# Kernel tuning notes

Measured on AMD Instinct MI355X. Metric: run time of the kernel, lower is better.

Reference implementation:

```python
import jax, jax.numpy as jnp
import numpy as np

NUM_HEADS = 16
HEAD_CH = 64
D_MODEL = 1024  # == NUM_HEADS*HEAD_CH -> out_mapper is Identity


def setup_inputs() -> dict:
    key = jax.random.key(0)
    k1, k2, k3 = jax.random.split(key, 3)
    tokens = jax.random.normal(k1, (2, 2048, D_MODEL), dtype=jnp.float32)
    w_qkv = jax.random.normal(k2, (D_MODEL, 3 * D_MODEL), dtype=jnp.float32) * (1.0 / np.sqrt(D_MODEL))
    b_qkv = jax.random.normal(k3, (3 * D_MODEL,), dtype=jnp.float32) * 0.02
    return {"tokens": tokens, "w_qkv": w_qkv, "b_qkv": b_qkv}


def reference(tokens, w_qkv, b_qkv):
    b, n, _ = tokens.shape
    qkv = tokens @ w_qkv + b_qkv  # [b, n, 3*inner]
    q, k, v = jnp.split(qkv, 3, axis=-1)

    def heads(x):  # [b, n, h*d] -> [b, h, n, d]
        return x.reshape(b, n, NUM_HEADS, HEAD_CH).transpose(0, 2, 1, 3)

    q, k, v = heads(q), heads(k), heads(v)
    scores = jnp.einsum('bhqd,bhkd->bhqk', q, k) / jnp.sqrt(jnp.float32(HEAD_CH))
    attn = jax.nn.softmax(scores, axis=-1)
    out = jnp.einsum('bhqk,bhkd->bhqd', attn, v)  # [b, h, n, d]
    out = out.transpose(0, 2, 1, 3).reshape(b, n, NUM_HEADS * HEAD_CH)
    return out  # out_mapper is Identity since inner_channels == input_channels
```

## Files before the change

kernel.cpp:

```cpp
#include <hip/hip_runtime.h>
#include <stdint.h>

typedef __attribute__((ext_vector_type(8))) short shortx8;
typedef __attribute__((ext_vector_type(4))) float floatx4;
typedef unsigned short bf16_t;

#define NH 16
#define HD 64
#define SEQ 2048
#define BATCH 2
#define DM 1024
#define DM3 3072

#define GLDS(gp, lp) __builtin_amdgcn_global_load_lds( \
    (const __attribute__((address_space(1))) unsigned int*)(gp), \
    (__attribute__((address_space(3))) unsigned int*)(lp), 16, 0, 0)

__device__ __forceinline__ bf16_t f2bf(float f) {
    unsigned int u = __float_as_uint(f);
    u += 0x7fff + ((u >> 16) & 1);
    return (bf16_t)(u >> 16);
}

__global__ __launch_bounds__(256) void conv_tokens(const float* __restrict__ in,
                                                   bf16_t* __restrict__ out) {
    int idx = blockIdx.x * 256 + threadIdx.x;
    float4 a = ((const float4*)in)[idx * 2];
    float4 b = ((const float4*)in)[idx * 2 + 1];
    uint4 o;
    o.x = (unsigned)f2bf(a.x) | ((unsigned)f2bf(a.y) << 16);
    o.y = (unsigned)f2bf(a.z) | ((unsigned)f2bf(a.w) << 16);
    o.z = (unsigned)f2bf(b.x) | ((unsigned)f2bf(b.y) << 16);
    o.w = (unsigned)f2bf(b.z) | ((unsigned)f2bf(b.w) << 16);
    ((uint4*)out)[idx] = o;
}

__global__ __launch_bounds__(256) void conv_w(const float* __restrict__ w,
                                              bf16_t* __restrict__ wt) {
    __shared__ bf16_t t[64 * 65];
    const int n0 = blockIdx.x * 64;
    const int k0 = blockIdx.y * 64;
    const int tid = threadIdx.x;
    for (int i = 0; i < 16; i++) {
        int idx = i * 256 + tid;
        int r = idx >> 6, c = idx & 63;
        t[r * 65 + c] = f2bf(w[(k0 + r) * DM3 + n0 + c]);
    }
    __syncthreads();
    for (int i = 0; i < 16; i++) {
        int idx = i * 256 + tid;
        int r = idx >> 6, c = idx & 63;
        wt[(n0 + r) * DM + k0 + c] = t[c * 65 + r];
    }
}


#define QSCALE 0.18033688011f
__global__ __launch_bounds__(256) void qkv_gemm(const bf16_t* __restrict__ A,
                                                const bf16_t* __restrict__ Bt,
                                                const float* __restrict__ bias,
                                                bf16_t* __restrict__ Qo,
                                                bf16_t* __restrict__ Ko,
                                                bf16_t* __restrict__ Vto) {
    __shared__ __align__(16) char smem[128 * 136 * 2];
    bf16_t* As = (bf16_t*)smem;
    bf16_t* Bs = As + 128 * 64;
    bf16_t* Cs = (bf16_t*)smem;
    const int m0 = blockIdx.x * 128;
    const int n0 = blockIdx.y * 128;
    const int tid = threadIdx.x;
    const int wave = tid >> 6, lane = tid & 63;
    const int quad = lane >> 4, l16 = lane & 15;
    const int wm = (wave & 1) * 64, wn = (wave >> 1) * 64;
    const int srow = tid >> 3;
    const int swz8 = ((tid & 7) ^ (srow & 7)) * 8;
    const int h3 = l16 & 7;
    floatx4 acc[4][4] = {};

    for (int kt = 0; kt < DM; kt += 64) {
        __syncthreads();
        for (int rr = 0; rr < 4; rr++) {
            GLDS(&A[(m0 + rr * 32 + srow) * DM + kt + swz8], &As[rr * 2048 + tid * 8]);
            GLDS(&Bt[(n0 + rr * 32 + srow) * DM + kt + swz8], &Bs[rr * 2048 + tid * 8]);
        }
        __syncthreads();
        for (int ks = 0; ks < 2; ks++) {
            const int g = ((ks * 4 + quad) ^ h3) * 8;
            shortx8 af[4], bfr[4];
            for (int t = 0; t < 4; t++)
                af[t] = *(const shortx8*)&As[(wm + t * 16 + l16) * 64 + g];
            for (int t = 0; t < 4; t++)
                bfr[t] = *(const shortx8*)&Bs[(wn + t * 16 + l16) * 64 + g];
            for (int i = 0; i < 4; i++)
                for (int j = 0; j < 4; j++)
                    acc[i][j] = __builtin_amdgcn_mfma_f32_16x16x32_bf16(af[i], bfr[j], acc[i][j], 0, 0, 0);
        }
    }

    const int part = n0 >> 10;
    const int b = m0 >> 11, pos0 = m0 & 2047;

    if (part != 2) {
        for (int i = 0; i < 4; i++)
            for (int j = 0; j < 4; j++)
                for (int r = 0; r < 4; r++) {
                    int m = m0 + wm + i * 16 + quad * 4 + r;
                    int n = n0 + wn + j * 16 + l16;
                    float v = acc[i][j][r] + bias[n];
                    int rr = n & 1023;
                    int h = rr >> 6, d = rr & 63;
                    int pos = m & 2047;
                    if (part == 0)
                        Qo[((b * NH + h) * SEQ + pos) * HD + d] = f2bf(v * QSCALE);
                    else
                        Ko[((b * NH + h) * SEQ + pos) * HD + d] = f2bf(v);
                }
    } else {
        __syncthreads();
        for (int i = 0; i < 4; i++)
            for (int j = 0; j < 4; j++) {
                int nl = wn + j * 16 + l16;
                int n = n0 + nl;
                float bv = bias[n];
                uint2 pk;
                pk.x = (unsigned)f2bf(acc[i][j][0] + bv) | ((unsigned)f2bf(acc[i][j][1] + bv) << 16);
                pk.y = (unsigned)f2bf(acc[i][j][2] + bv) | ((unsigned)f2bf(acc[i][j][3] + bv) << 16);
                *(uint2*)&Cs[nl * 136 + wm + i * 16 + quad * 4] = pk;
            }
        __syncthreads();
        for (int p = 0; p < 8; p++) {
            int nl = p * 16 + (tid >> 4);
            int g = tid & 15;
            uint4 v = *(const uint4*)&Cs[nl * 136 + g * 8];
            int rr = (n0 + nl) & 1023;
            int h = rr >> 6, d = rr & 63;
            *(uint4*)&Vto[(size_t)((b * NH + h) * HD + d) * SEQ + pos0 + g * 8] = v;
        }
    }
}

__global__ __launch_bounds__(256, 2) void attn(const bf16_t* __restrict__ Q,
                                               const bf16_t* __restrict__ K,
                                               const bf16_t* __restrict__ Vt,
                                               float* __restrict__ out) {
    __shared__ __align__(16) char smem[65536];
    bf16_t* Ks = (bf16_t*)smem;
    bf16_t* Vs = (bf16_t*)(smem + 16384);
    bf16_t* Ps = (bf16_t*)(smem + 32768);

    const int qt_blk = blockIdx.x;
    const int bh = blockIdx.y;
    const int b = bh >> 4, h = bh & 15;
    const int q0 = qt_blk * 128;
    const bf16_t* Qb = Q + ((size_t)bh * SEQ + q0) * HD;
    const bf16_t* Kb = K + (size_t)bh * SEQ * HD;
    const bf16_t* Vb = Vt + (size_t)bh * HD * SEQ;
    const int tid = threadIdx.x;
    const int wave = tid >> 6, lane = tid & 63;
    const int quad = lane >> 4, l16 = lane & 15;
    const int h3 = l16 & 7;
    const int qh = wave >> 1, kh = wave & 1;
    bf16_t* Pw = Ps + wave * 4096;

    const int srow = tid >> 3;
    const int sg8 = ((tid & 7) ^ (srow & 7)) * 8;
    const int vrow = tid >> 4;
    const int vg8 = (((tid & 15) ^ vrow) & 15) * 8;

    shortx8 qf[4][2];
    for (int qt = 0; qt < 4; qt++)
        for (int kc = 0; kc < 2; kc++)
            qf[qt][kc] = *(const shortx8*)&Qb[(qh * 64 + qt * 16 + l16) * 64 + kc * 32 + quad * 8];

    float m_i[4] = {-1e30f, -1e30f, -1e30f, -1e30f};
    float l_i[4] = {0.f, 0.f, 0.f, 0.f};
    floatx4 acc_o[4][4] = {};

    for (int it = 0; it < SEQ / 128; ++it) {
        const int k0 = it * 128;
        for (int rr = 0; rr < 4; rr++) {
            GLDS(&Kb[(k0 + rr * 32 + srow) * 64 + sg8], &Ks[rr * 2048 + tid * 8]);
            GLDS(&Vb[(size_t)(rr * 16 + vrow) * SEQ + k0 + vg8], &Vs[rr * 2048 + tid * 8]);
        }
        __syncthreads();

        floatx4 s[4][4] = {};
        for (int kc = 0; kc < 2; kc++) {
            const int g = ((kc * 4 + quad) ^ h3) * 8;
            shortx8 kf[4];
            for (int kt = 0; kt < 4; kt++)
                kf[kt] = *(const shortx8*)&Ks[(kh * 64 + kt * 16 + l16) * 64 + g];
            for (int kt = 0; kt < 4; kt++)
                for (int qt = 0; qt < 4; qt++)
                    s[kt][qt] = __builtin_amdgcn_mfma_f32_16x16x32_bf16(kf[kt], qf[qt][kc], s[kt][qt], 0, 0, 0);
        }

        for (int qt = 0; qt < 4; qt++) {
            float mx = -1e30f;
            for (int kt = 0; kt < 4; kt++)
                for (int r = 0; r < 4; r++) mx = fmaxf(mx, s[kt][qt][r]);
            mx = fmaxf(mx, __shfl_xor(mx, 16, 64));
            mx = fmaxf(mx, __shfl_xor(mx, 32, 64));
            float mnew = fmaxf(m_i[qt], mx);
            float al = __builtin_amdgcn_exp2f(m_i[qt] - mnew);
            m_i[qt] = mnew;
            float rs = 0.f;
            for (int kt = 0; kt < 4; kt++) {
                unsigned u[4];
                for (int r = 0; r < 4; r++) {
                    float p = __builtin_amdgcn_exp2f(s[kt][qt][r] - mnew);
                    rs += p;
                    u[r] = __float_as_uint(p) + 0x8000u;
                }
                uint2 pk;
                pk.x = __builtin_amdgcn_perm(u[1], u[0], 0x07060302u);
                pk.y = __builtin_amdgcn_perm(u[3], u[2], 0x07060302u);
                *(uint2*)&Pw[(qt * 16 + l16) * 64 +
                             ((2 * kt + (quad >> 1)) ^ h3) * 8 + (quad & 1) * 4] = pk;
            }
            rs += __shfl_xor(rs, 16, 64);
            rs += __shfl_xor(rs, 32, 64);
            l_i[qt] = l_i[qt] * al + rs;
            if (__any(al < 1.0f))
                for (int dt = 0; dt < 4; dt++)
                    for (int r = 0; r < 4; r++) acc_o[dt][qt][r] *= al;
        }

        for (int kc = 0; kc < 2; kc++) {
            const int gp = ((kc * 4 + quad) ^ h3) * 8;
            shortx8 vf[4], pf[4];
            for (int qt = 0; qt < 4; qt++)
                pf[qt] = *(const shortx8*)&Pw[(qt * 16 + l16) * 64 + gp];
            for (int dt = 0; dt < 4; dt++)
                vf[dt] = *(const shortx8*)&Vs[(dt * 16 + l16) * 128 +
                                              (((kh * 8 + kc * 4 + quad) ^ l16) & 15) * 8];
            for (int dt = 0; dt < 4; dt++)
                for (int qt = 0; qt < 4; qt++)
                    acc_o[dt][qt] = __builtin_amdgcn_mfma_f32_16x16x32_bf16(vf[dt], pf[qt], acc_o[dt][qt], 0, 0, 0);
        }
        __syncthreads();
    }

    float* Osh = (float*)smem;
    float* ml = (float*)(smem + 64512);
    if (kh == 1) {
        for (int qt = 0; qt < 4; qt++) {
            for (int dt = 0; dt < 4; dt++) {
                float4 o;
                o.x = acc_o[dt][qt][0]; o.y = acc_o[dt][qt][1];
                o.z = acc_o[dt][qt][2]; o.w = acc_o[dt][qt][3];
                *(float4*)&Osh[qh * 4096 + (qt * 16 + l16) * 64 +
                               (((dt * 4 + quad) ^ l16) & 15) * 4] = o;
            }
            if (quad == 0) {
                ml[(qh * 4 + qt) * 32 + l16] = m_i[qt];
                ml[(qh * 4 + qt) * 32 + 16 + l16] = l_i[qt];
            }
        }
    }
    __syncthreads();
    if (kh == 0) {
        for (int qt = 0; qt < 4; qt++) {
            float m1 = ml[(qh * 4 + qt) * 32 + l16];
            float l1 = ml[(qh * 4 + qt) * 32 + 16 + l16];
            float m = fmaxf(m_i[qt], m1);
            float a0 = __builtin_amdgcn_exp2f(m_i[qt] - m);
            float a1 = __builtin_amdgcn_exp2f(m1 - m);
            float inv = 1.0f / (l_i[qt] * a0 + l1 * a1);
            int q = q0 + qh * 64 + qt * 16 + l16;
            for (int dt = 0; dt < 4; dt++) {
                float4 o1 = *(const float4*)&Osh[qh * 4096 + (qt * 16 + l16) * 64 +
                                                 (((dt * 4 + quad) ^ l16) & 15) * 4];
                float4 o;
                o.x = (acc_o[dt][qt][0] * a0 + o1.x * a1) * inv;
                o.y = (acc_o[dt][qt][1] * a0 + o1.y * a1) * inv;
                o.z = (acc_o[dt][qt][2] * a0 + o1.z * a1) * inv;
                o.w = (acc_o[dt][qt][3] * a0 + o1.w * a1) * inv;
                *(float4*)&out[(size_t)(b * SEQ + q) * DM + h * HD + dt * 16 + quad * 4] = o;
            }
        }
    }
}

extern "C" void kernel_launch(void* const* d_in, const int* in_sizes, int n_in,
                              void* d_out, int out_size, void* d_ws, size_t ws_size,
                              hipStream_t stream) {
    const float* tokens = (const float*)d_in[0];
    const float* w = (const float*)d_in[1];
    const float* bias = (const float*)d_in[2];
    float* out = (float*)d_out;
    char* ws = (char*)d_ws;

    bf16_t* tok_bf = (bf16_t*)(ws);
    bf16_t* wt_bf  = (bf16_t*)(ws + (size_t)8 * 1024 * 1024);
    bf16_t* Qb     = (bf16_t*)(ws + (size_t)14 * 1024 * 1024);
    bf16_t* Kb     = (bf16_t*)(ws + (size_t)22 * 1024 * 1024);
    bf16_t* Vb     = (bf16_t*)(ws + (size_t)30 * 1024 * 1024);

    conv_tokens<<<2048, 256, 0, stream>>>(tokens, tok_bf);
    conv_w<<<dim3(48, 16), 256, 0, stream>>>(w, wt_bf);
    qkv_gemm<<<dim3(32, 24), 256, 0, stream>>>(tok_bf, wt_bf, bias, Qb, Kb, Vb);
    attn<<<dim3(16, 32), 256, 0, stream>>>(Qb, Kb, Vb, out);
}
```

Before: 181.3 us.

## Merge conversion kernels, vectorize QKV epilogue, and drop LDS staging in attention

The two conversion kernels become one launch. The Q/K GEMM epilogue swaps the MFMA operands so each lane writes four packed bf16 values with a vector bias load, replacing scalar stores. The attention kernel stops staging K and V through LDS and loads MFMA fragments directly from global memory, removing the per-iteration barriers. It also adds a lazy max-rescale threshold that skips most accumulator rescales, and raises occupancy hints to three blocks. The risks are uncoalesced or redundant global reads of K and V across waves, plus a small numeric change from the deferred max update.

```diff
diff --git a/kernel.cpp b/kernel.cpp
--- a/kernel.cpp
+++ b/kernel.cpp
@@ -22,40 +22,76 @@
     return (bf16_t)(u >> 16);
 }
 
-__global__ __launch_bounds__(256) void conv_tokens(const float* __restrict__ in,
-                                                   bf16_t* __restrict__ out) {
-    int idx = blockIdx.x * 256 + threadIdx.x;
-    float4 a = ((const float4*)in)[idx * 2];
-    float4 b = ((const float4*)in)[idx * 2 + 1];
-    uint4 o;
-    o.x = (unsigned)f2bf(a.x) | ((unsigned)f2bf(a.y) << 16);
-    o.y = (unsigned)f2bf(a.z) | ((unsigned)f2bf(a.w) << 16);
-    o.z = (unsigned)f2bf(b.x) | ((unsigned)f2bf(b.y) << 16);
-    o.w = (unsigned)f2bf(b.z) | ((unsigned)f2bf(b.w) << 16);
-    ((uint4*)out)[idx] = o;
-}
-
-__global__ __launch_bounds__(256) void conv_w(const float* __restrict__ w,
-                                              bf16_t* __restrict__ wt) {
+__global__ __launch_bounds__(256) void conv_all(const float* __restrict__ tokens,
+                                                bf16_t* __restrict__ tok_bf,
+                                                const float* __restrict__ w,
+                                                bf16_t* __restrict__ wt) {
     __shared__ bf16_t t[64 * 65];
-    const int n0 = blockIdx.x * 64;
-    const int k0 = blockIdx.y * 64;
+    const int bx = blockIdx.x, tid = threadIdx.x;
+    if (bx < 2048) {
+        int idx = bx * 256 + tid;
+        float4 a = ((const float4*)tokens)[idx * 2];
+        float4 b = ((const float4*)tokens)[idx * 2 + 1];
+        uint4 o;
+        o.x = (unsigned)f2bf(a.x) | ((unsigned)f2bf(a.y) << 16);
+        o.y = (unsigned)f2bf(a.z) | ((unsigned)f2bf(a.w) << 16);
+        o.z = (unsigned)f2bf(b.x) | ((unsigned)f2bf(b.y) << 16);
+        o.w = (unsigned)f2bf(b.z) | ((unsigned)f2bf(b.w) << 16);
+        ((uint4*)tok_bf)[idx] = o;
+    } else {
+        const int bw = bx - 2048;
+        const int n0 = (bw % 48) * 64, k0 = (bw / 48) * 64;
+        for (int i = 0; i < 16; i++) {
+            int idx = i * 256 + tid;
+            int r = idx >> 6, c = idx & 63;
+            t[r * 65 + c] = f2bf(w[(k0 + r) * DM3 + n0 + c]);
+        }
+        __syncthreads();
+        for (int i = 0; i < 16; i++) {
+            int idx = i * 256 + tid;
+            int r = idx >> 6, c = idx & 63;
+            wt[(n0 + r) * DM + k0 + c] = t[c * 65 + r];
+        }
+    }
+}
+
+
+#define QSCALE 0.18033688011f
+
+template<bool SW>
+__device__ __forceinline__ void kloop(const bf16_t* __restrict__ A, const bf16_t* __restrict__ Bt,
+                                      bf16_t* __restrict__ As, bf16_t* __restrict__ Bs,
+                                      int m0, int n0, floatx4 (&acc)[4][4]) {
     const int tid = threadIdx.x;
-    for (int i = 0; i < 16; i++) {
-        int idx = i * 256 + tid;
-        int r = idx >> 6, c = idx & 63;
-        t[r * 65 + c] = f2bf(w[(k0 + r) * DM3 + n0 + c]);
-    }
-    __syncthreads();
-    for (int i = 0; i < 16; i++) {
-        int idx = i * 256 + tid;
-        int r = idx >> 6, c = idx & 63;
-        wt[(n0 + r) * DM + k0 + c] = t[c * 65 + r];
-    }
-}
-
-
-#define QSCALE 0.18033688011f
+    const int wave = tid >> 6, lane = tid & 63;
+    const int quad = lane >> 4, l16 = lane & 15;
+    const int wm = (wave & 1) * 64, wn = (wave >> 1) * 64;
+    const int srow = tid >> 3;
+    const int swz8 = ((tid & 7) ^ (srow & 7)) * 8;
+    const int h3 = l16 & 7;
+    for (int kt = 0; kt < DM; kt += 64) {
+        __syncthreads();
+        for (int rr = 0; rr < 4; rr++) {
+            GLDS(&A[(m0 + rr * 32 + srow) * DM + kt + swz8], &As[rr * 2048 + tid * 8]);
+            GLDS(&Bt[(n0 + rr * 32 + srow) * DM + kt + swz8], &Bs[rr * 2048 + tid * 8]);
+        }
+        __syncthreads();
+        for (int ks = 0; ks < 2; ks++) {
+            const int g = ((ks * 4 + quad) ^ h3) * 8;
+            shortx8 af[4], bfr[4];
+            for (int t = 0; t < 4; t++)
+                af[t] = *(const shortx8*)&As[(wm + t * 16 + l16) * 64 + g];
+            for (int t = 0; t < 4; t++)
+                bfr[t] = *(const shortx8*)&Bs[(wn + t * 16 + l16) * 64 + g];
+            for (int i = 0; i < 4; i++)
+                for (int j = 0; j < 4; j++)
+                    acc[i][j] = SW
+                        ? __builtin_amdgcn_mfma_f32_16x16x32_bf16(bfr[j], af[i], acc[i][j], 0, 0, 0)
+                        : __builtin_amdgcn_mfma_f32_16x16x32_bf16(af[i], bfr[j], acc[i][j], 0, 0, 0);
+        }
+    }
+}
+
 __global__ __launch_bounds__(256) void qkv_gemm(const bf16_t* __restrict__ A,
                                                 const bf16_t* __restrict__ Bt,
                                                 const float* __restrict__ bias,
@@ -72,56 +108,37 @@
     const int wave = tid >> 6, lane = tid & 63;
     const int quad = lane >> 4, l16 = lane & 15;
     const int wm = (wave & 1) * 64, wn = (wave >> 1) * 64;
-    const int srow = tid >> 3;
-    const int swz8 = ((tid & 7) ^ (srow & 7)) * 8;
-    const int h3 = l16 & 7;
-    floatx4 acc[4][4] = {};
-
-    for (int kt = 0; kt < DM; kt += 64) {
-        __syncthreads();
-        for (int rr = 0; rr < 4; rr++) {
-            GLDS(&A[(m0 + rr * 32 + srow) * DM + kt + swz8], &As[rr * 2048 + tid * 8]);
-            GLDS(&Bt[(n0 + rr * 32 + srow) * DM + kt + swz8], &Bs[rr * 2048 + tid * 8]);
-        }
-        __syncthreads();
-        for (int ks = 0; ks < 2; ks++) {
-            const int g = ((ks * 4 + quad) ^ h3) * 8;
-            shortx8 af[4], bfr[4];
-            for (int t = 0; t < 4; t++)
-                af[t] = *(const shortx8*)&As[(wm + t * 16 + l16) * 64 + g];
-            for (int t = 0; t < 4; t++)
-                bfr[t] = *(const shortx8*)&Bs[(wn + t * 16 + l16) * 64 + g];
-            for (int i = 0; i < 4; i++)
-                for (int j = 0; j < 4; j++)
-                    acc[i][j] = __builtin_amdgcn_mfma_f32_16x16x32_bf16(af[i], bfr[j], acc[i][j], 0, 0, 0);
-        }
-    }
-
     const int part = n0 >> 10;
     const int b = m0 >> 11, pos0 = m0 & 2047;
+    floatx4 acc[4][4] = {};
 
     if (part != 2) {
-        for (int i = 0; i < 4; i++)
-            for (int j = 0; j < 4; j++)
-                for (int r = 0; r < 4; r++) {
-                    int m = m0 + wm + i * 16 + quad * 4 + r;
-                    int n = n0 + wn + j * 16 + l16;
-                    float v = acc[i][j][r] + bias[n];
-                    int rr = n & 1023;
-                    int h = rr >> 6, d = rr & 63;
-                    int pos = m & 2047;
-                    if (part == 0)
-                        Qo[((b * NH + h) * SEQ + pos) * HD + d] = f2bf(v * QSCALE);
-                    else
-                        Ko[((b * NH + h) * SEQ + pos) * HD + d] = f2bf(v);
-                }
+        kloop<true>(A, Bt, As, Bs, m0, n0, acc);
+        for (int i = 0; i < 4; i++) {
+            int m = m0 + wm + i * 16 + l16;
+            int pos = m & 2047;
+            for (int j = 0; j < 4; j++) {
+                int nb = n0 + wn + j * 16 + quad * 4;
+                float4 bv = *(const float4*)&bias[nb];
+                float v0 = acc[i][j][0] + bv.x, v1 = acc[i][j][1] + bv.y;
+                float v2 = acc[i][j][2] + bv.z, v3 = acc[i][j][3] + bv.w;
+                if (part == 0) { v0 *= QSCALE; v1 *= QSCALE; v2 *= QSCALE; v3 *= QSCALE; }
+                uint2 pk;
+                pk.x = (unsigned)f2bf(v0) | ((unsigned)f2bf(v1) << 16);
+                pk.y = (unsigned)f2bf(v2) | ((unsigned)f2bf(v3) << 16);
+                int rr = nb & 1023;
+                int h = rr >> 6, d = rr & 63;
+                bf16_t* dst = (part == 0) ? Qo : Ko;
+                *(uint2*)&dst[(size_t)((b * NH + h) * SEQ + pos) * HD + d] = pk;
+            }
+        }
     } else {
+        kloop<false>(A, Bt, As, Bs, m0, n0, acc);
         __syncthreads();
         for (int i = 0; i < 4; i++)
             for (int j = 0; j < 4; j++) {
                 int nl = wn + j * 16 + l16;
-                int n = n0 + nl;
-                float bv = bias[n];
+                float bv = bias[n0 + nl];
                 uint2 pk;
                 pk.x = (unsigned)f2bf(acc[i][j][0] + bv) | ((unsigned)f2bf(acc[i][j][1] + bv) << 16);
                 pk.y = (unsigned)f2bf(acc[i][j][2] + bv) | ((unsigned)f2bf(acc[i][j][3] + bv) << 16);
@@ -139,15 +156,12 @@
     }
 }
 
-__global__ __launch_bounds__(256, 2) void attn(const bf16_t* __restrict__ Q,
+__global__ __launch_bounds__(256, 3) void attn(const bf16_t* __restrict__ Q,
                                                const bf16_t* __restrict__ K,
                                                const bf16_t* __restrict__ Vt,
                                                float* __restrict__ out) {
-    __shared__ __align__(16) char smem[65536];
-    bf16_t* Ks = (bf16_t*)smem;
-    bf16_t* Vs = (bf16_t*)(smem + 16384);
-    bf16_t* Ps = (bf16_t*)(smem + 32768);
-
+    __shared__ __align__(16) bf16_t Ps[4][4096];
+    __shared__ float ml[256];
     const int qt_blk = blockIdx.x;
     const int bh = blockIdx.y;
     const int b = bh >> 4, h = bh & 15;
@@ -160,40 +174,29 @@
     const int quad = lane >> 4, l16 = lane & 15;
     const int h3 = l16 & 7;
     const int qh = wave >> 1, kh = wave & 1;
-    bf16_t* Pw = Ps + wave * 4096;
-
-    const int srow = tid >> 3;
-    const int sg8 = ((tid & 7) ^ (srow & 7)) * 8;
-    const int vrow = tid >> 4;
-    const int vg8 = (((tid & 15) ^ vrow) & 15) * 8;
+    bf16_t* Pw = Ps[wave];
 
     shortx8 qf[4][2];
     for (int qt = 0; qt < 4; qt++)
         for (int kc = 0; kc < 2; kc++)
             qf[qt][kc] = *(const shortx8*)&Qb[(qh * 64 + qt * 16 + l16) * 64 + kc * 32 + quad * 8];
 
-    float m_i[4] = {-1e30f, -1e30f, -1e30f, -1e30f};
+    float m_app[4] = {-1e30f, -1e30f, -1e30f, -1e30f};
     float l_i[4] = {0.f, 0.f, 0.f, 0.f};
     floatx4 acc_o[4][4] = {};
 
     for (int it = 0; it < SEQ / 128; ++it) {
         const int k0 = it * 128;
-        for (int rr = 0; rr < 4; rr++) {
-            GLDS(&Kb[(k0 + rr * 32 + srow) * 64 + sg8], &Ks[rr * 2048 + tid * 8]);
-            GLDS(&Vb[(size_t)(rr * 16 + vrow) * SEQ + k0 + vg8], &Vs[rr * 2048 + tid * 8]);
-        }
-        __syncthreads();
-
+        shortx8 kfa[2][4];
+        for (int kc = 0; kc < 2; kc++)
+            for (int kt = 0; kt < 4; kt++)
+                kfa[kc][kt] = *(const shortx8*)&Kb[(size_t)(k0 + kh * 64 + kt * 16 + l16) * 64 +
+                                                   kc * 32 + quad * 8];
         floatx4 s[4][4] = {};
-        for (int kc = 0; kc < 2; kc++) {
-            const int g = ((kc * 4 + quad) ^ h3) * 8;
-            shortx8 kf[4];
-            for (int kt = 0; kt < 4; kt++)
-                kf[kt] = *(const shortx8*)&Ks[(kh * 64 + kt * 16 + l16) * 64 + g];
+        for (int kc = 0; kc < 2; kc++)
             for (int kt = 0; kt < 4; kt++)
                 for (int qt = 0; qt < 4; qt++)
-                    s[kt][qt] = __builtin_amdgcn_mfma_f32_16x16x32_bf16(kf[kt], qf[qt][kc], s[kt][qt], 0, 0, 0);
-        }
+                    s[kt][qt] = __builtin_amdgcn_mfma_f32_16x16x32_bf16(kfa[kc][kt], qf[qt][kc], s[kt][qt], 0, 0, 0);
 
         for (int qt = 0; qt < 4; qt++) {
             float mx = -1e30f;
@@ -201,14 +204,19 @@
                 for (int r = 0; r < 4; r++) mx = fmaxf(mx, s[kt][qt][r]);
             mx = fmaxf(mx, __shfl_xor(mx, 16, 64));
             mx = fmaxf(mx, __shfl_xor(mx, 32, 64));
-            float mnew = fmaxf(m_i[qt], mx);
-            float al = __builtin_amdgcn_exp2f(m_i[qt] - mnew);
-            m_i[qt] = mnew;
+            float d = m_app[qt] - mx;
+            if (__any(d < -0.415f)) {
+                float al = __builtin_amdgcn_exp2f(fminf(d, 0.f));
+                l_i[qt] *= al;
+                for (int dt = 0; dt < 4; dt++)
+                    for (int r = 0; r < 4; r++) acc_o[dt][qt][r] *= al;
+                m_app[qt] = fmaxf(m_app[qt], mx);
+            }
             float rs = 0.f;
             for (int kt = 0; kt < 4; kt++) {
                 unsigned u[4];
                 for (int r = 0; r < 4; r++) {
-                    float p = __builtin_amdgcn_exp2f(s[kt][qt][r] - mnew);
+                    float p = __builtin_amdgcn_exp2f(s[kt][qt][r] - m_app[qt]);
                     rs += p;
                     u[r] = __float_as_uint(p) + 0x8000u;
                 }
@@ -220,29 +228,25 @@
             }
             rs += __shfl_xor(rs, 16, 64);
             rs += __shfl_xor(rs, 32, 64);
-            l_i[qt] = l_i[qt] * al + rs;
-            if (__any(al < 1.0f))
-                for (int dt = 0; dt < 4; dt++)
-                    for (int r = 0; r < 4; r++) acc_o[dt][qt][r] *= al;
+            l_i[qt] += rs;
         }
 
         for (int kc = 0; kc < 2; kc++) {
             const int gp = ((kc * 4 + quad) ^ h3) * 8;
             shortx8 vf[4], pf[4];
+            for (int dt = 0; dt < 4; dt++)
+                vf[dt] = *(const shortx8*)&Vb[(size_t)(dt * 16 + l16) * SEQ +
+                                              k0 + kh * 64 + kc * 32 + quad * 8];
             for (int qt = 0; qt < 4; qt++)
                 pf[qt] = *(const shortx8*)&Pw[(qt * 16 + l16) * 64 + gp];
             for (int dt = 0; dt < 4; dt++)
-                vf[dt] = *(const shortx8*)&Vs[(dt * 16 + l16) * 128 +
-                                              (((kh * 8 + kc * 4 + quad) ^ l16) & 15) * 8];
-            for (int dt = 0; dt < 4; dt++)
                 for (int qt = 0; qt < 4; qt++)
                     acc_o[dt][qt] = __builtin_amdgcn_mfma_f32_16x16x32_bf16(vf[dt], pf[qt], acc_o[dt][qt], 0, 0, 0);
         }
-        __syncthreads();
-    }
-
-    float* Osh = (float*)smem;
-    float* ml = (float*)(smem + 64512);
+    }
+
+    float* Osh = (float*)Ps;
+    __syncthreads();
     if (kh == 1) {
         for (int qt = 0; qt < 4; qt++) {
             for (int dt = 0; dt < 4; dt++) {
@@ -253,7 +257,7 @@
                                (((dt * 4 + quad) ^ l16) & 15) * 4] = o;
             }
             if (quad == 0) {
-                ml[(qh * 4 + qt) * 32 + l16] = m_i[qt];
+                ml[(qh * 4 + qt) * 32 + l16] = m_app[qt];
                 ml[(qh * 4 + qt) * 32 + 16 + l16] = l_i[qt];
             }
         }
@@ -263,8 +267,8 @@
         for (int qt = 0; qt < 4; qt++) {
             float m1 = ml[(qh * 4 + qt) * 32 + l16];
             float l1 = ml[(qh * 4 + qt) * 32 + 16 + l16];
-            float m = fmaxf(m_i[qt], m1);
-            float a0 = __builtin_amdgcn_exp2f(m_i[qt] - m);
+            float m = fmaxf(m_app[qt], m1);
+            float a0 = __builtin_amdgcn_exp2f(m_app[qt] - m);
             float a1 = __builtin_amdgcn_exp2f(m1 - m);
             float inv = 1.0f / (l_i[qt] * a0 + l1 * a1);
             int q = q0 + qh * 64 + qt * 16 + l16;
@@ -297,8 +301,7 @@
     bf16_t* Kb     = (bf16_t*)(ws + (size_t)22 * 1024 * 1024);
     bf16_t* Vb     = (bf16_t*)(ws + (size_t)30 * 1024 * 1024);
 
-    conv_tokens<<<2048, 256, 0, stream>>>(tokens, tok_bf);
-    conv_w<<<dim3(48, 16), 256, 0, stream>>>(w, wt_bf);
+    conv_all<<<2816, 256, 0, stream>>>(tokens, tok_bf, w, wt_bf);
     qkv_gemm<<<dim3(32, 24), 256, 0, stream>>>(tok_bf, wt_bf, bias, Qb, Kb, Vb);
     attn<<<dim3(16, 32), 256, 0, stream>>>(Qb, Kb, Vb, out);
 }
```

Result: slower. 272.8 us (+50.4%).
